# Performance work log

Measured on AMD Instinct MI355X. Metric: run time of the kernel, lower is better.

## Reference

```python
import jax, jax.numpy as jnp
import numpy as np

B, C, H, W = 2, 32, 512, 512
EMB = 10            # emb_dim
LW = 64             # linear_layer_width
BANDS = (EMB - 2) // 4


def _pos_axis(n):
    # PositionalEmbedding2D per-axis embedding: [t, Re(z), Im(z)] -> [n, 1+2*bands]
    t = np.linspace(0.0, 1.0, n)[:, None]
    tr = np.linspace(0.0, n - 1.0, n)[:, None]
    w = 2.0 * np.pi * tr / n
    f = np.linspace(1e-4, BANDS - 1.0, BANDS)[None, :]
    z = np.exp(-1j * f * w)
    return np.concatenate([t, z.real, z.imag], axis=-1).astype(np.float32)


def setup_inputs() -> dict:
    key = jax.random.key(0)
    ks = jax.random.split(key, 6)
    s = 0.02
    return {
        "u": jax.random.normal(ks[0], (B, C, H, W), dtype=jnp.float32),
        "z_height": jnp.asarray(_pos_axis(H)),  # [H, EMB//2], trainable pos-emb param
        "z_width": jnp.asarray(_pos_axis(W)),   # [W, EMB//2]
        "W0": jax.random.normal(ks[1], (EMB, LW), dtype=jnp.float32) * s,
        "b0": jnp.zeros((LW,), dtype=jnp.float32),
        "W1": jax.random.normal(ks[2], (LW, LW), dtype=jnp.float32) * s,
        "b1": jnp.zeros((LW,), dtype=jnp.float32),
        "W2": jax.random.normal(ks[3], (LW, LW), dtype=jnp.float32) * s,
        "b2": jnp.zeros((LW,), dtype=jnp.float32),
        "Wout": jax.random.normal(ks[4], (LW, C), dtype=jnp.float32) * s,
        "freq": jnp.ones((LW,), dtype=jnp.float32),          # Sin2D freq, w=1 (shared act)
        "deltas": jnp.linspace(0.1, 0.3, C, dtype=jnp.float32),  # GaussianModulation2D sigmas
        "D": jax.random.normal(ks[5], (C,), dtype=jnp.float32),  # self.bias
    }


def reference(u, z_height, z_width, W0, b0, W1, b1, W2, b2, Wout, freq, deltas, D):
    # --- implicit filter: 2D grid positional embedding [H, W, EMB] ---
    zh = jnp.broadcast_to(z_height[:, None, :], (H, W, EMB // 2))
    zw = jnp.broadcast_to(z_width[None, :, :], (H, W, EMB // 2))
    z = jnp.concatenate([zh, zw], axis=-1)
    sin = lambda x: jnp.sin(freq * x)  # shared Sin2D activation
    h = sin(z @ W0 + b0)
    h = sin(h @ W1 + b1)               # num_inner_mlps = 2
    h = sin(h @ W2 + b2)
    h = h @ Wout                       # [H, W, C], final Linear has no bias
    # --- Gaussian modulation (note: code centers x by width/2, y by height/2) ---
    xg = (jnp.arange(H, dtype=jnp.float32) - W / 2.0)[:, None]
    yg = (jnp.arange(W, dtype=jnp.float32) - H / 2.0)[None, :]
    r2 = xg * xg + yg * yg             # [H, W]
    scalers = (1.0 / (deltas * jnp.sqrt(2.0 * jnp.pi))) * jnp.exp(
        -0.5 * (r2[..., None] / deltas) ** 2
    )
    k = (h * scalers).transpose(2, 0, 1)  # [C, H, W]
    # --- fftconv2d: zero-padded 2D FFT long conv + elementwise bias path ---
    FH, FW = 2 * H, 2 * W
    k_f = jnp.fft.rfftn(k, s=(FH, FW), axes=(1, 2)) / (FH * FW)  # [C, FH, FW//2+1]
    u_f = jnp.fft.rfftn(u, s=(FH, FW), axes=(2, 3))              # [B, C, FH, FW//2+1]
    y = jnp.fft.irfftn(u_f * k_f[None], s=(FH, FW), axes=(2, 3))[..., :H, :W]
    return (y + u * D[None, :, None, None]).astype(u.dtype)
```

## Files before the change

kernel.cpp:

```cpp
#include <hip/hip_runtime.h>
#include <hip/hip_bf16.h>
#include <math.h>


#define HDIM 512
#define WDIM 512
#define CDIM 32
#define BDIM 2
#define HW   (HDIM*WDIM)
#define NBLOCK 2048

__global__ __launch_bounds__(64) void compute_taps_kernel(
    const float* __restrict__ zh,
    const float* __restrict__ zw,
    const float* __restrict__ W0,
    const float* __restrict__ b0,
    const float* __restrict__ W1,
    const float* __restrict__ b1,
    const float* __restrict__ W2,
    const float* __restrict__ b2,
    const float* __restrict__ Wout,
    const float* __restrict__ freq,
    const float* __restrict__ deltas,
    float* __restrict__ taps)
{
    int p = blockIdx.x;
    int o = threadIdx.x;
    int di = p / 3 - 1;
    int dj = p % 3 - 1;
    int i = 256 + di;
    int j = 256 + dj;

    __shared__ float sh[64];

    float z[10];
    #pragma unroll
    for (int e = 0; e < 5; e++) z[e]     = zh[i * 5 + e];
    #pragma unroll
    for (int e = 0; e < 5; e++) z[5 + e] = zw[j * 5 + e];

    float f = freq[o];

    float acc = b0[o];
    #pragma unroll
    for (int e = 0; e < 10; e++) acc += z[e] * W0[e * 64 + o];
    float h = sinf(f * acc);
    sh[o] = h;
    __syncthreads();

    acc = b1[o];
    #pragma unroll 8
    for (int e = 0; e < 64; e++) acc += sh[e] * W1[e * 64 + o];
    h = sinf(f * acc);
    __syncthreads();
    sh[o] = h;
    __syncthreads();

    acc = b2[o];
    #pragma unroll 8
    for (int e = 0; e < 64; e++) acc += sh[e] * W2[e * 64 + o];
    h = sinf(f * acc);
    __syncthreads();
    sh[o] = h;
    __syncthreads();

    if (o < 32) {
        float ho = 0.0f;
        #pragma unroll 8
        for (int e = 0; e < 64; e++) ho += sh[e] * Wout[e * 32 + o];
        float delta = deltas[o];
        float r2 = (float)(di * di + dj * dj);
        float q = r2 / delta;
        float scaler = expf(-0.5f * q * q) / (delta * 2.5066282746310002f);
        taps[p * 32 + o] = ho * scaler * (1.0f / (1024.0f * 1024.0f));
    }
}

__global__ __launch_bounds__(256) void hyena_main_kernel(
    const float* __restrict__ u,
    const float* __restrict__ D,
    const float* __restrict__ taps,
    float* __restrict__ out)
{
    const int block = blockIdx.x;
    const int bc  = block >> 5;
    const int c   = bc & 31;
    const int sub = (block + bc) & 31;
    const int t   = threadIdx.x;

    const int chunk = (bc << 5) | sub;
    const int g0  = (chunk << 11) + t;
    const float* __restrict__ up = u + (g0 << 2);

    float4 v[8];
    #pragma unroll
    for (int k = 0; k < 8; ++k)
        v[k] = *reinterpret_cast<const float4*>(up + (k << 10));

    const float d = D[c];
    #pragma unroll
    for (int k = 0; k < 8; ++k) {
        v[k].x *= d; v[k].y *= d; v[k].z *= d; v[k].w *= d;
    }

    const int j0     = (t & 127) << 2;
    const int i_base = (sub << 4) + (t >> 7);
    if (sub >= 15 && j0 >= 252) {
        float tp[9];
        #pragma unroll
        for (int p = 0; p < 9; ++p) tp[p] = taps[p * 32 + c];

        const float* __restrict__ ubase = u + bc * HW;
        #pragma unroll
        for (int k = 0; k < 8; ++k) {
            int i = i_base + (k << 1);
            if (i < 255) continue;
            #pragma unroll
            for (int a = 0; a < 3; ++a) {
                int si = i - 255 - a;
                if (si < 0) continue;
                const float* row = ubase + si * WDIM;
                float w[6];
                w[0] = (j0 >= 260) ? row[j0 - 257] : 0.0f;
                if (j0 >= 256) {
                    const float4 Bv = *reinterpret_cast<const float4*>(row + j0 - 256);
                    w[1] = Bv.x; w[2] = Bv.y; w[3] = Bv.z; w[4] = Bv.w;
                } else {
                    w[1] = w[2] = w[3] = w[4] = 0.0f;
                }
                w[5] = row[j0 - 252];
                #pragma unroll
                for (int bb = 0; bb < 3; ++bb) {
                    float tv = tp[a * 3 + bb];
                    v[k].x += tv * w[2 - bb + 0];
                    v[k].y += tv * w[2 - bb + 1];
                    v[k].z += tv * w[2 - bb + 2];
                    v[k].w += tv * w[2 - bb + 3];
                }
            }
        }
    }

    float* __restrict__ op = out + (g0 << 2);
    #pragma unroll
    for (int k = 0; k < 8; ++k)
        *reinterpret_cast<float4*>(op + (k << 10)) = v[k];
}

extern "C" void kernel_launch(void* const* d_in, const int* in_sizes, int n_in,
                              void* d_out, int out_size, void* d_ws, size_t ws_size,
                              hipStream_t stream) {
    const float* u      = (const float*)d_in[0];
    const float* zh     = (const float*)d_in[1];
    const float* zw     = (const float*)d_in[2];
    const float* W0     = (const float*)d_in[3];
    const float* b0     = (const float*)d_in[4];
    const float* W1     = (const float*)d_in[5];
    const float* b1     = (const float*)d_in[6];
    const float* W2     = (const float*)d_in[7];
    const float* b2     = (const float*)d_in[8];
    const float* Wout   = (const float*)d_in[9];
    const float* freq   = (const float*)d_in[10];
    const float* deltas = (const float*)d_in[11];
    const float* D      = (const float*)d_in[12];
    float* out  = (float*)d_out;
    float* taps = (float*)d_ws;

    compute_taps_kernel<<<9, 64, 0, stream>>>(zh, zw, W0, b0, W1, b1, W2, b2,
                                              Wout, freq, deltas, taps);
    hyena_main_kernel<<<NBLOCK, 256, 0, stream>>>(u, D, taps, out);
}
```

Baseline: 150.3 us.

## Overlap tap MLP with pure-scale blocks and split conv blocks into second kernel

```diff
diff --git a/kernel.cpp b/kernel.cpp
--- a/kernel.cpp
+++ b/kernel.cpp
@@ -8,9 +8,11 @@
 #define CDIM 32
 #define BDIM 2
 #define HW   (HDIM*WDIM)
-#define NBLOCK 2048
 
-__global__ __launch_bounds__(64) void compute_taps_kernel(
+typedef float f4v __attribute__((ext_vector_type(4)));
+
+__global__ __launch_bounds__(256) void hyena_stream_taps_kernel(
+    const float* __restrict__ u,
     const float* __restrict__ zh,
     const float* __restrict__ zw,
     const float* __restrict__ W0,
@@ -22,90 +24,106 @@
     const float* __restrict__ Wout,
     const float* __restrict__ freq,
     const float* __restrict__ deltas,
+    const float* __restrict__ D,
+    float* __restrict__ out,
     float* __restrict__ taps)
 {
-    int p = blockIdx.x;
-    int o = threadIdx.x;
-    int di = p / 3 - 1;
-    int dj = p % 3 - 1;
-    int i = 256 + di;
-    int j = 256 + dj;
+    const int block = blockIdx.x;
+    const int t = threadIdx.x;
 
-    __shared__ float sh[64];
+    if (block == 960) {
+        __shared__ float HA[576];
+        __shared__ float HB[576];
+        for (int n = t; n < 576; n += 256) {
+            int p = n >> 6, o = n & 63;
+            int di = p / 3 - 1, dj = p % 3 - 1;
+            float acc = b0[o];
+            #pragma unroll
+            for (int e = 0; e < 5; e++) acc += zh[(256 + di) * 5 + e] * W0[e * 64 + o];
+            #pragma unroll
+            for (int e = 0; e < 5; e++) acc += zw[(256 + dj) * 5 + e] * W0[(5 + e) * 64 + o];
+            HA[n] = sinf(freq[o] * acc);
+        }
+        __syncthreads();
+        for (int n = t; n < 576; n += 256) {
+            int p = n >> 6, o = n & 63;
+            float acc = b1[o];
+            #pragma unroll 8
+            for (int e = 0; e < 64; e++) acc += HA[(p << 6) + e] * W1[e * 64 + o];
+            HB[n] = sinf(freq[o] * acc);
+        }
+        __syncthreads();
+        for (int n = t; n < 576; n += 256) {
+            int p = n >> 6, o = n & 63;
+            float acc = b2[o];
+            #pragma unroll 8
+            for (int e = 0; e < 64; e++) acc += HB[(p << 6) + e] * W2[e * 64 + o];
+            HA[n] = sinf(freq[o] * acc);
+        }
+        __syncthreads();
+        if (t < 288) {
+            int p = t >> 5, c = t & 31;
+            int di = p / 3 - 1, dj = p % 3 - 1;
+            float acc = 0.0f;
+            #pragma unroll 8
+            for (int e = 0; e < 64; e++) acc += HA[(p << 6) + e] * Wout[e * 32 + c];
+            float delta = deltas[c];
+            float r2 = (float)(di * di + dj * dj);
+            float q = r2 / delta;
+            float scaler = expf(-0.5f * q * q) / (delta * 2.5066282746310002f);
+            taps[p * 32 + c] = acc * scaler * (1.0f / (1024.0f * 1024.0f));
+        }
+        return;
+    }
 
-    float z[10];
+    const int bc  = block / 15;
+    const int sub = block - bc * 15;
+    const int c   = bc & 31;
+    const int chunk = (bc << 5) | sub;
+    const int g0  = (chunk << 11) + t;
+    const float* __restrict__ up = u + (g0 << 2);
+
+    f4v v[8];
     #pragma unroll
-    for (int e = 0; e < 5; e++) z[e]     = zh[i * 5 + e];
+    for (int k = 0; k < 8; ++k)
+        v[k] = *reinterpret_cast<const f4v*>(up + (k << 10));
+
+    const float d = D[c];
+    float* __restrict__ op = out + (g0 << 2);
     #pragma unroll
-    for (int e = 0; e < 5; e++) z[5 + e] = zw[j * 5 + e];
-
-    float f = freq[o];
-
-    float acc = b0[o];
-    #pragma unroll
-    for (int e = 0; e < 10; e++) acc += z[e] * W0[e * 64 + o];
-    float h = sinf(f * acc);
-    sh[o] = h;
-    __syncthreads();
-
-    acc = b1[o];
-    #pragma unroll 8
-    for (int e = 0; e < 64; e++) acc += sh[e] * W1[e * 64 + o];
-    h = sinf(f * acc);
-    __syncthreads();
-    sh[o] = h;
-    __syncthreads();
-
-    acc = b2[o];
-    #pragma unroll 8
-    for (int e = 0; e < 64; e++) acc += sh[e] * W2[e * 64 + o];
-    h = sinf(f * acc);
-    __syncthreads();
-    sh[o] = h;
-    __syncthreads();
-
-    if (o < 32) {
-        float ho = 0.0f;
-        #pragma unroll 8
-        for (int e = 0; e < 64; e++) ho += sh[e] * Wout[e * 32 + o];
-        float delta = deltas[o];
-        float r2 = (float)(di * di + dj * dj);
-        float q = r2 / delta;
-        float scaler = expf(-0.5f * q * q) / (delta * 2.5066282746310002f);
-        taps[p * 32 + o] = ho * scaler * (1.0f / (1024.0f * 1024.0f));
-    }
+    for (int k = 0; k < 8; ++k)
+        __builtin_nontemporal_store(v[k] * d, reinterpret_cast<f4v*>(op + (k << 10)));
 }
 
-__global__ __launch_bounds__(256) void hyena_main_kernel(
+__global__ __launch_bounds__(256) void hyena_conv_kernel(
     const float* __restrict__ u,
     const float* __restrict__ D,
     const float* __restrict__ taps,
     float* __restrict__ out)
 {
     const int block = blockIdx.x;
-    const int bc  = block >> 5;
+    const int bc  = block / 17;
+    const int sub = 15 + (block - bc * 17);
     const int c   = bc & 31;
-    const int sub = (block + bc) & 31;
     const int t   = threadIdx.x;
 
     const int chunk = (bc << 5) | sub;
     const int g0  = (chunk << 11) + t;
     const float* __restrict__ up = u + (g0 << 2);
 
-    float4 v[8];
+    f4v v[8];
     #pragma unroll
     for (int k = 0; k < 8; ++k)
-        v[k] = *reinterpret_cast<const float4*>(up + (k << 10));
+        v[k] = *reinterpret_cast<const f4v*>(up + (k << 10));
 
     const float d = D[c];
     #pragma unroll
-    for (int k = 0; k < 8; ++k) {
-        v[k].x *= d; v[k].y *= d; v[k].z *= d; v[k].w *= d;
-    }
+    for (int k = 0; k < 8; ++k)
+        v[k] *= d;
 
     const int j0     = (t & 127) << 2;
     const int i_base = (sub << 4) + (t >> 7);
-    if (sub >= 15 && j0 >= 252) {
+    if (j0 >= 252) {
         float tp[9];
         #pragma unroll
         for (int p = 0; p < 9; ++p) tp[p] = taps[p * 32 + c];
@@ -123,7 +141,7 @@
                 float w[6];
                 w[0] = (j0 >= 260) ? row[j0 - 257] : 0.0f;
                 if (j0 >= 256) {
-                    const float4 Bv = *reinterpret_cast<const float4*>(row + j0 - 256);
+                    const f4v Bv = *reinterpret_cast<const f4v*>(row + j0 - 256);
                     w[1] = Bv.x; w[2] = Bv.y; w[3] = Bv.z; w[4] = Bv.w;
                 } else {
                     w[1] = w[2] = w[3] = w[4] = 0.0f;
@@ -144,7 +162,7 @@
     float* __restrict__ op = out + (g0 << 2);
     #pragma unroll
     for (int k = 0; k < 8; ++k)
-        *reinterpret_cast<float4*>(op + (k << 10)) = v[k];
+        __builtin_nontemporal_store(v[k], reinterpret_cast<f4v*>(op + (k << 10)));
 }
 
 extern "C" void kernel_launch(void* const* d_in, const int* in_sizes, int n_in,
@@ -166,7 +184,8 @@
     float* out  = (float*)d_out;
     float* taps = (float*)d_ws;
 
-    compute_taps_kernel<<<9, 64, 0, stream>>>(zh, zw, W0, b0, W1, b1, W2, b2,
-                                              Wout, freq, deltas, taps);
-    hyena_main_kernel<<<NBLOCK, 256, 0, stream>>>(u, D, taps, out);
+    hyena_stream_taps_kernel<<<961, 256, 0, stream>>>(u, zh, zw, W0, b0, W1, b1,
+                                                      W2, b2, Wout, freq, deltas,
+                                                      D, out, taps);
+    hyena_conv_kernel<<<1088, 256, 0, stream>>>(u, D, taps, out);
 }
```

Result: slower. 157.1 us (+4.5%).
